# Kernel optimization log

Hardware: AMD Instinct MI355X
Metric: run time of the kernel (lower is better)

The kernel has to match this reference:

```python
import jax, jax.numpy as jnp
import numpy as np
from jax import lax

LAM = 1.0
B, L = 64, 512
WORD_DIM, POS_DIM, HIDDEN = 256, 32, 768
D_E = 3 * WORD_DIM            # 768, Xe feature dim
D_P = 2 * POS_DIM + WORD_DIM  # 320, Xp feature dim

# fixed piecewise-pool mask table: row 0 = padding, rows 1..3 = segments
MASK_TABLE = jnp.array([[0, 0, 0], [1, 0, 0], [0, 1, 0], [0, 0, 1]], dtype=jnp.float32)


def setup_inputs() -> dict:
    key = jax.random.key(0)
    ks = jax.random.split(key, 9)
    s1 = 1.0 / np.sqrt(D_E)
    s2 = 1.0 / np.sqrt(D_P)
    sc = 1.0 / np.sqrt(D_E * 3)
    return {
        "Xp": jax.random.normal(ks[0], (B, L, D_P), jnp.float32),
        "Xe": jax.random.normal(ks[1], (B, L, D_E), jnp.float32),
        "X_mask": jax.random.randint(ks[2], (B, L), 0, 4, jnp.int32),
        "W1": jax.random.uniform(ks[3], (D_E, D_E), jnp.float32, -s1, s1),
        "b1": jax.random.uniform(ks[4], (D_E,), jnp.float32, -s1, s1),
        "W2": jax.random.uniform(ks[5], (D_E, D_P), jnp.float32, -s2, s2),
        "b2": jax.random.uniform(ks[6], (D_E,), jnp.float32, -s2, s2),
        "Wc": jax.random.uniform(ks[7], (HIDDEN, D_E, 3), jnp.float32, -sc, sc),
        "bc": jax.random.uniform(ks[8], (HIDDEN,), jnp.float32, -sc, sc),
    }


def _forward(Xp, Xe, W1, b1, W2, b2, Wc, bc, X_mask):
    # gated linear fusion of entity and position features
    A = jax.nn.sigmoid(jnp.einsum('bld,od->blo', Xe / LAM, W1) + b1)   # [B,L,D_E]
    X = A * Xe + (1.0 - A) * jnp.tanh(jnp.einsum('bld,od->blo', Xp, W2) + b2)
    # conv1d over length, padding=1 (same)
    x_ncl = jnp.transpose(X, (0, 2, 1))                                 # [B,D_E,L]
    y = lax.conv_general_dilated(x_ncl, Wc, window_strides=(1,),
                                 padding=((1, 1),),
                                 dimension_numbers=('NCH', 'OIH', 'NCH'))
    y = jnp.transpose(y + bc[None, :, None], (0, 2, 1))                 # [B,L,H]
    # piecewise max pooling: mask-multiply then max over L, per segment
    m = MASK_TABLE[X_mask]                                              # [B,L,3]
    pooled = jnp.stack([jnp.max(y * m[:, :, k:k + 1], axis=1) for k in range(3)],
                       axis=-1)                                         # [B,H,3]
    return jnp.tanh(pooled.reshape(-1, HIDDEN * 3))                     # [B,3H]


def reference(Xp, Xe, X_mask, W1, b1, W2, b2, Wc, bc):
    return _forward(Xp, Xe, W1, b1, W2, b2, Wc, bc, X_mask)
```

## Files before the change

kernel.cpp:

```cpp
#include <hip/hip_runtime.h>
#include <math.h>

#define DE 768
#define DP 320
#define HID 768
#define LL 512
#define BB 64
#define M_TOT (BB * LL)
#define HD (HID * DE)

typedef _Float16 half8 __attribute__((ext_vector_type(8)));
typedef _Float16 half4 __attribute__((ext_vector_type(4)));
typedef _Float16 half2v __attribute__((ext_vector_type(2)));
typedef float floatx4 __attribute__((ext_vector_type(4)));

__device__ __forceinline__ void gload16(const void* g, void* l) {
    __builtin_amdgcn_global_load_lds(
        (const __attribute__((address_space(1))) unsigned int*)g,
        (__attribute__((address_space(3))) unsigned int*)l, 16, 0, 0);
}

__device__ __forceinline__ float fast_sigmoid(float x) {
    return __builtin_amdgcn_rcpf(1.f + __expf(-x));
}
__device__ __forceinline__ float fast_tanh(float x) {
    return 2.f * __builtin_amdgcn_rcpf(1.f + __expf(-2.f * x)) - 1.f;
}

__device__ __forceinline__ unsigned fkey(float v) {
    unsigned u = __float_as_uint(v);
    return (u & 0x80000000u) ? ~u : (u | 0x80000000u);
}
__device__ __forceinline__ float funkey(unsigned k) {
    unsigned u = (k & 0x80000000u) ? (k & 0x7FFFFFFFu) : ~k;
    return __uint_as_float(u);
}

__global__ __launch_bounds__(256) void prep_all(
    const float* __restrict__ Xe, const float* __restrict__ W1,
    const float* __restrict__ W2, const float* __restrict__ Wc,
    _Float16* __restrict__ Xe_h, _Float16* __restrict__ W1_h,
    _Float16* __restrict__ W2_h, _Float16* __restrict__ WcT)
{
    const int bid = blockIdx.x, tid = threadIdx.x;
    if (bid < 24576) {
        int idx = bid * 256 + tid;
        float4 v = ((const float4*)Xe)[idx];
        half4 h = {(_Float16)v.x, (_Float16)v.y, (_Float16)v.z, (_Float16)v.w};
        *(half4*)&Xe_h[(size_t)idx * 4] = h;
    } else if (bid < 25152) {
        int idx = (bid - 24576) * 256 + tid;
        float4 v = ((const float4*)W1)[idx];
        half4 h = {(_Float16)v.x, (_Float16)v.y, (_Float16)v.z, (_Float16)v.w};
        *(half4*)&W1_h[(size_t)idx * 4] = h;
    } else if (bid < 25392) {
        int idx = (bid - 25152) * 256 + tid;
        float4 v = ((const float4*)W2)[idx];
        half4 h = {(_Float16)v.x, (_Float16)v.y, (_Float16)v.z, (_Float16)v.w};
        *(half4*)&W2_h[(size_t)idx * 4] = h;
    } else {
        int idx = (bid - 25392) * 256 + tid;
        float a = Wc[(size_t)idx * 3 + 0];
        float b = Wc[(size_t)idx * 3 + 1];
        float c = Wc[(size_t)idx * 3 + 2];
        WcT[idx]          = (_Float16)a;
        WcT[HD + idx]     = (_Float16)b;
        WcT[2 * HD + idx] = (_Float16)c;
    }
}

__global__ __launch_bounds__(256) void gate_kernel(
    const _Float16* __restrict__ Xe_h, const float* __restrict__ Xp,
    const _Float16* __restrict__ W1_h, const float* __restrict__ b1,
    const _Float16* __restrict__ W2_h, const float* __restrict__ b2,
    _Float16* __restrict__ Xout)
{
    __shared__ __align__(16) char smem[24576];
    _Float16 (*As)[32] = (_Float16 (*)[32])smem;
    float    (*Af)[32] = (float (*)[32])smem;
    _Float16 (*Bs)[32] = (_Float16 (*)[32])(smem + 16384);
    unsigned (*Ep)[132] = (unsigned (*)[132])smem;

    const int tid = threadIdx.x;
    const int lane = tid & 63, wid = tid >> 6;
    const int quad = lane >> 4, l15 = lane & 15;
    const int wm = (wid & 1) * 64, wn = (wid >> 1) * 64;
    const int m0 = blockIdx.y * 128, n0 = blockIdx.x * 128;
    const int i4 = lane >> 2, c8 = (lane & 3) * 8;
    const int c8x = c8 ^ ((i4 & 3) * 8);
    const int i8 = lane >> 3, c4 = (lane & 7) * 4;
    const int c4x = c4 ^ ((i8 & 3) * 8);
    const int rsw = (l15 & 3) * 8;

    floatx4 acc[4][4] = {};

    for (int k0 = 0; k0 < DP; k0 += 32) {
        __syncthreads();
        #pragma unroll
        for (int t = 0; t < 4; ++t) {
            int rb = wid * 32 + t * 8;
            gload16(&Xp[(size_t)(m0 + rb + i8) * DP + k0 + c4x], &Af[rb][0]);
        }
        #pragma unroll
        for (int t = 0; t < 2; ++t) {
            int rb = wid * 32 + t * 16;
            gload16(&W2_h[(size_t)(n0 + rb + i4) * DP + k0 + c8x], &Bs[rb][0]);
        }
        __syncthreads();
        half8 af[4], bf[4];
        #pragma unroll
        for (int i = 0; i < 4; ++i) {
            int row = wm + i * 16 + l15;
            int sb = (quad * 8) ^ rsw;
            float4 x0 = *(float4*)&Af[row][sb];
            float4 x1 = *(float4*)&Af[row][sb + 4];
            half8 h = {(_Float16)x0.x, (_Float16)x0.y, (_Float16)x0.z, (_Float16)x0.w,
                       (_Float16)x1.x, (_Float16)x1.y, (_Float16)x1.z, (_Float16)x1.w};
            af[i] = h;
        }
        #pragma unroll
        for (int j = 0; j < 4; ++j)
            bf[j] = *(half8*)&Bs[wn + j * 16 + l15][(quad * 8) ^ rsw];
        #pragma unroll
        for (int i = 0; i < 4; ++i)
            #pragma unroll
            for (int j = 0; j < 4; ++j)
                acc[i][j] = __builtin_amdgcn_mfma_f32_16x16x32_f16(af[i], bf[j], acc[i][j], 0, 0, 0);
    }

    half4 tpk[4][4];
    #pragma unroll
    for (int j = 0; j < 4; ++j) {
        float b2v = b2[n0 + wn + j * 16 + l15];
        #pragma unroll
        for (int i = 0; i < 4; ++i) {
            half4 h;
            #pragma unroll
            for (int r = 0; r < 4; ++r)
                h[r] = (_Float16)fast_tanh(acc[i][j][r] + b2v);
            tpk[i][j] = h;
            acc[i][j] = (floatx4){0.f, 0.f, 0.f, 0.f};
        }
    }

    for (int k0 = 0; k0 < DE; k0 += 32) {
        __syncthreads();
        #pragma unroll
        for (int t = 0; t < 2; ++t) {
            int rb = wid * 32 + t * 16;
            gload16(&Xe_h[(size_t)(m0 + rb + i4) * DE + k0 + c8x], &As[rb][0]);
            gload16(&W1_h[(size_t)(n0 + rb + i4) * DE + k0 + c8x], &Bs[rb][0]);
        }
        __syncthreads();
        half8 af[4], bf[4];
        #pragma unroll
        for (int i = 0; i < 4; ++i)
            af[i] = *(half8*)&As[wm + i * 16 + l15][(quad * 8) ^ rsw];
        #pragma unroll
        for (int j = 0; j < 4; ++j)
            bf[j] = *(half8*)&Bs[wn + j * 16 + l15][(quad * 8) ^ rsw];
        #pragma unroll
        for (int i = 0; i < 4; ++i)
            #pragma unroll
            for (int j = 0; j < 4; ++j)
                acc[i][j] = __builtin_amdgcn_mfma_f32_16x16x32_f16(af[i], bf[j], acc[i][j], 0, 0, 0);
    }

    float b1v[4];
    #pragma unroll
    for (int j = 0; j < 4; ++j) b1v[j] = b1[n0 + wn + j * 16 + l15];

    #pragma unroll
    for (int p = 0; p < 4; ++p) {
        __syncthreads();
        if ((wm >> 6) == (p >> 1)) {
            #pragma unroll
            for (int ii = 0; ii < 2; ++ii) {
                int i = (p & 1) * 2 + ii;
                #pragma unroll
                for (int j = 0; j < 4; ++j) {
                    int col = wn + j * 16 + l15;
                    #pragma unroll
                    for (int r = 0; r < 4; ++r) {
                        int row_l = ii * 16 + quad * 4 + r;
                        float g = fast_sigmoid(acc[i][j][r] + b1v[j]);
                        half2v gt;
                        gt[0] = (_Float16)g;
                        gt[1] = tpk[i][j][r];
                        Ep[row_l][col] = __builtin_bit_cast(unsigned, gt);
                    }
                }
            }
        }
        __syncthreads();
        #pragma unroll
        for (int q = 0; q < 4; ++q) {
            int row_l = q * 8 + (tid >> 5);
            int col = (tid & 31) * 4;
            uint4 w = *(const uint4*)&Ep[row_l][col];
            size_t goff = (size_t)(m0 + p * 32 + row_l) * DE + n0 + col;
            half4 xe4 = *(const half4*)&Xe_h[goff];
            half4 r4;
            #pragma unroll
            for (int e = 0; e < 4; ++e) {
                half2v gt = __builtin_bit_cast(half2v, (&w.x)[e]);
                float g = (float)gt[0], t = (float)gt[1];
                float xe = (float)xe4[e];
                r4[e] = (_Float16)(g * xe + (1.f - g) * t);
            }
            *(half4*)&Xout[goff] = r4;
        }
    }
}

__global__ __launch_bounds__(256) void conv_pool_kernel(
    const _Float16* __restrict__ X, const _Float16* __restrict__ WcT,
    const float* __restrict__ bc, const int* __restrict__ mask,
    unsigned* __restrict__ pool)
{
    __shared__ __align__(16) _Float16 As[144][32];
    __shared__ __align__(16) _Float16 Bs[3][128][32];
    __shared__ unsigned lpool[384];
    __shared__ int smask[128];
    __shared__ int anyNot[3];

    const int tid = threadIdx.x;
    const int lane = tid & 63, wid = tid >> 6;
    const int quad = lane >> 4, l15 = lane & 15;
    const int wm = (wid & 1) * 64, wn = (wid >> 1) * 64;
    const int m0 = blockIdx.y * 128, n0 = blockIdx.x * 128;
    const int b = m0 >> 9, l0 = m0 & 511;
    const int i4 = lane >> 2, c8 = (lane & 3) * 8;
    const int c8x = c8 ^ ((i4 & 3) * 8);
    const int rsw = (l15 & 3) * 8;

    if (tid < 3) anyNot[tid] = 0;
    for (int i = tid; i < 384; i += 256) lpool[i] = 0u;
    if (tid < 128) smask[tid] = mask[b * LL + l0 + tid];
    if (l0 == 0   && tid < 4) *(uint4*)&As[7][tid * 8]   = make_uint4(0u, 0u, 0u, 0u);
    if (l0 == 384 && tid < 4) *(uint4*)&As[136][tid * 8] = make_uint4(0u, 0u, 0u, 0u);
    __syncthreads();
    if (tid < 128) {
        int mv = smask[tid];
        if (mv != 1) atomicOr(&anyNot[0], 1);
        if (mv != 2) atomicOr(&anyNot[1], 1);
        if (mv != 3) atomicOr(&anyNot[2], 1);
    }

    floatx4 acc[4][4] = {};
    for (int k0 = 0; k0 < DE; k0 += 32) {
        __syncthreads();
        #pragma unroll
        for (int t = 0; t < 2; ++t) {
            int c = wid + t * 4;
            int g = l0 - 8 + c * 16 + i4;
            if ((unsigned)g < (unsigned)LL)
                gload16(&X[((size_t)b * LL + g) * DE + k0 + c8x], &As[c * 16][0]);
        }
        if (wid == 0) {
            int g = l0 + 120 + i4;
            if ((unsigned)g < (unsigned)LL)
                gload16(&X[((size_t)b * LL + g) * DE + k0 + c8x], &As[128][0]);
        }
        #pragma unroll
        for (int s = 0; s < 3; ++s) {
            #pragma unroll
            for (int t = 0; t < 2; ++t) {
                int rb = wid * 32 + t * 16;
                gload16(&WcT[(size_t)s * HD + (size_t)(n0 + rb + i4) * DE + k0 + c8x],
                        &Bs[s][rb][0]);
            }
        }
        __syncthreads();
        #pragma unroll
        for (int s = 0; s < 3; ++s) {
            half8 af[4], bf[4];
            #pragma unroll
            for (int i = 0; i < 4; ++i) {
                int pr = wm + i * 16 + l15 + s + 7;
                af[i] = *(half8*)&As[pr][(quad * 8) ^ ((pr & 3) * 8)];
            }
            #pragma unroll
            for (int j = 0; j < 4; ++j)
                bf[j] = *(half8*)&Bs[s][wn + j * 16 + l15][(quad * 8) ^ rsw];
            #pragma unroll
            for (int i = 0; i < 4; ++i)
                #pragma unroll
                for (int j = 0; j < 4; ++j)
                    acc[i][j] = __builtin_amdgcn_mfma_f32_16x16x32_f16(af[i], bf[j], acc[i][j], 0, 0, 0);
        }
    }

    float tmax[4][3];
    #pragma unroll
    for (int j = 0; j < 4; ++j)
        #pragma unroll
        for (int sg = 0; sg < 3; ++sg) tmax[j][sg] = -1e38f;

    #pragma unroll
    for (int i = 0; i < 4; ++i) {
        #pragma unroll
        for (int r = 0; r < 4; ++r) {
            int ll = wm + i * 16 + quad * 4 + r;
            int seg = smask[ll] - 1;
            if (seg >= 0) {
                #pragma unroll
                for (int j = 0; j < 4; ++j)
                    tmax[j][seg] = fmaxf(tmax[j][seg], acc[i][j][r]);
            }
        }
    }
    #pragma unroll
    for (int j = 0; j < 4; ++j) {
        int h = wn + j * 16 + l15;
        float bias = bc[n0 + h];
        #pragma unroll
        for (int sg = 0; sg < 3; ++sg)
            if (tmax[j][sg] > -1e37f)
                atomicMax(&lpool[h * 3 + sg], fkey(tmax[j][sg] + bias));
    }
    __syncthreads();
    for (int i = tid; i < 384; i += 256) {
        int hl = i / 3, k = i - hl * 3;
        unsigned key = lpool[i];
        if (anyNot[k]) {
            unsigned z = fkey(0.0f);
            if (z > key) key = z;
        }
        atomicMax(&pool[((size_t)b * HID + n0 + hl) * 3 + k], key);
    }
}

__global__ void finish_k(const unsigned* __restrict__ pool, float* __restrict__ out) {
    int idx = blockIdx.x * blockDim.x + threadIdx.x;
    if (idx < BB * HID * 3) out[idx] = tanhf(funkey(pool[idx]));
}

extern "C" void kernel_launch(void* const* d_in, const int* in_sizes, int n_in,
                              void* d_out, int out_size, void* d_ws, size_t ws_size,
                              hipStream_t stream) {
    const float* Xp = (const float*)d_in[0];
    const float* Xe = (const float*)d_in[1];
    const int*   Xm = (const int*)d_in[2];
    const float* W1 = (const float*)d_in[3];
    const float* b1 = (const float*)d_in[4];
    const float* W2 = (const float*)d_in[5];
    const float* b2 = (const float*)d_in[6];
    const float* Wc = (const float*)d_in[7];
    const float* bc = (const float*)d_in[8];
    float* out = (float*)d_out;

    _Float16* Xe_h = (_Float16*)d_ws;
    _Float16* X_h  = Xe_h + (size_t)M_TOT * DE;
    _Float16* W1_h = X_h + (size_t)M_TOT * DE;
    _Float16* W2_h = W1_h + (size_t)DE * DE;
    _Float16* WcT  = W2_h + (size_t)DE * DP;
    unsigned* pool = (unsigned*)(WcT + (size_t)3 * HD);

    hipMemsetAsync(pool, 0, (size_t)BB * HID * 3 * sizeof(unsigned), stream);
    prep_all<<<27696, 256, 0, stream>>>(Xe, W1, W2, Wc, Xe_h, W1_h, W2_h, WcT);
    gate_kernel<<<dim3(DE / 128, M_TOT / 128), 256, 0, stream>>>(
        Xe_h, Xp, W1_h, b1, W2_h, b2, X_h);
    conv_pool_kernel<<<dim3(HID / 128, M_TOT / 128), 256, 0, stream>>>(
        X_h, WcT, bc, Xm, pool);
    finish_k<<<(BB * HID * 3 + 255) / 256, 256, 0, stream>>>(pool, out);
}
```

Before: 457.8 us.

## Drop Xe fp16 prepass, remap blocks per XCD, enlarge conv tile to 256 rows

Removes the separate Xe fp32-to-fp16 conversion pass. The gate kernel now loads fp32 Xe straight into LDS and converts it while building fragments, with a new swizzle for fp32 tiles. Block indices are remapped so neighbouring M tiles land on the same XCD, which should improve L2 reuse of weights and activations. The conv/pool kernel grows to 512 threads with a 256-row M tile, so each weight tile is reused across more rows and fewer blocks merge results through atomics. In exchange, the gate kernel moves twice the bytes through LDS for its Xe operand, and the conv kernel needs more LDS per block.

```diff
diff --git a/kernel.cpp b/kernel.cpp
--- a/kernel.cpp
+++ b/kernel.cpp
@@ -36,30 +36,25 @@
     return __uint_as_float(u);
 }
 
-__global__ __launch_bounds__(256) void prep_all(
-    const float* __restrict__ Xe, const float* __restrict__ W1,
-    const float* __restrict__ W2, const float* __restrict__ Wc,
-    _Float16* __restrict__ Xe_h, _Float16* __restrict__ W1_h,
-    _Float16* __restrict__ W2_h, _Float16* __restrict__ WcT)
+__global__ __launch_bounds__(256) void prep_w(
+    const float* __restrict__ W1, const float* __restrict__ W2,
+    const float* __restrict__ Wc,
+    _Float16* __restrict__ W1_h, _Float16* __restrict__ W2_h,
+    _Float16* __restrict__ WcT)
 {
     const int bid = blockIdx.x, tid = threadIdx.x;
-    if (bid < 24576) {
+    if (bid < 576) {
         int idx = bid * 256 + tid;
-        float4 v = ((const float4*)Xe)[idx];
-        half4 h = {(_Float16)v.x, (_Float16)v.y, (_Float16)v.z, (_Float16)v.w};
-        *(half4*)&Xe_h[(size_t)idx * 4] = h;
-    } else if (bid < 25152) {
-        int idx = (bid - 24576) * 256 + tid;
         float4 v = ((const float4*)W1)[idx];
         half4 h = {(_Float16)v.x, (_Float16)v.y, (_Float16)v.z, (_Float16)v.w};
         *(half4*)&W1_h[(size_t)idx * 4] = h;
-    } else if (bid < 25392) {
-        int idx = (bid - 25152) * 256 + tid;
+    } else if (bid < 816) {
+        int idx = (bid - 576) * 256 + tid;
         float4 v = ((const float4*)W2)[idx];
         half4 h = {(_Float16)v.x, (_Float16)v.y, (_Float16)v.z, (_Float16)v.w};
         *(half4*)&W2_h[(size_t)idx * 4] = h;
     } else {
-        int idx = (bid - 25392) * 256 + tid;
+        int idx = (bid - 816) * 256 + tid;
         float a = Wc[(size_t)idx * 3 + 0];
         float b = Wc[(size_t)idx * 3 + 1];
         float c = Wc[(size_t)idx * 3 + 2];
@@ -70,13 +65,12 @@
 }
 
 __global__ __launch_bounds__(256) void gate_kernel(
-    const _Float16* __restrict__ Xe_h, const float* __restrict__ Xp,
+    const float* __restrict__ Xe, const float* __restrict__ Xp,
     const _Float16* __restrict__ W1_h, const float* __restrict__ b1,
     const _Float16* __restrict__ W2_h, const float* __restrict__ b2,
     _Float16* __restrict__ Xout)
 {
     __shared__ __align__(16) char smem[24576];
-    _Float16 (*As)[32] = (_Float16 (*)[32])smem;
     float    (*Af)[32] = (float (*)[32])smem;
     _Float16 (*Bs)[32] = (_Float16 (*)[32])(smem + 16384);
     unsigned (*Ep)[132] = (unsigned (*)[132])smem;
@@ -85,11 +79,14 @@
     const int lane = tid & 63, wid = tid >> 6;
     const int quad = lane >> 4, l15 = lane & 15;
     const int wm = (wid & 1) * 64, wn = (wid >> 1) * 64;
-    const int m0 = blockIdx.y * 128, n0 = blockIdx.x * 128;
+    const int linear = blockIdx.y * 6 + blockIdx.x;
+    const int xcd = linear & 7, kk = linear >> 3;
+    const int n0 = (kk % 6) * 128;
+    const int m0 = (xcd * 32 + kk / 6) * 128;
     const int i4 = lane >> 2, c8 = (lane & 3) * 8;
     const int c8x = c8 ^ ((i4 & 3) * 8);
     const int i8 = lane >> 3, c4 = (lane & 7) * 4;
-    const int c4x = c4 ^ ((i8 & 3) * 8);
+    const int c4x = c4 ^ ((i8 & 7) * 4);
     const int rsw = (l15 & 3) * 8;
 
     floatx4 acc[4][4] = {};
@@ -110,10 +107,9 @@
         half8 af[4], bf[4];
         #pragma unroll
         for (int i = 0; i < 4; ++i) {
-            int row = wm + i * 16 + l15;
-            int sb = (quad * 8) ^ rsw;
-            float4 x0 = *(float4*)&Af[row][sb];
-            float4 x1 = *(float4*)&Af[row][sb + 4];
+            int row = wm + i * 16 + l15, r7 = row & 7;
+            float4 x0 = *(float4*)&Af[row][((2 * quad) ^ r7) * 4];
+            float4 x1 = *(float4*)&Af[row][((2 * quad + 1) ^ r7) * 4];
             half8 h = {(_Float16)x0.x, (_Float16)x0.y, (_Float16)x0.z, (_Float16)x0.w,
                        (_Float16)x1.x, (_Float16)x1.y, (_Float16)x1.z, (_Float16)x1.w};
             af[i] = h;
@@ -146,16 +142,26 @@
     for (int k0 = 0; k0 < DE; k0 += 32) {
         __syncthreads();
         #pragma unroll
+        for (int t = 0; t < 4; ++t) {
+            int rb = wid * 32 + t * 8;
+            gload16(&Xe[(size_t)(m0 + rb + i8) * DE + k0 + c4x], &Af[rb][0]);
+        }
+        #pragma unroll
         for (int t = 0; t < 2; ++t) {
             int rb = wid * 32 + t * 16;
-            gload16(&Xe_h[(size_t)(m0 + rb + i4) * DE + k0 + c8x], &As[rb][0]);
             gload16(&W1_h[(size_t)(n0 + rb + i4) * DE + k0 + c8x], &Bs[rb][0]);
         }
         __syncthreads();
         half8 af[4], bf[4];
         #pragma unroll
-        for (int i = 0; i < 4; ++i)
-            af[i] = *(half8*)&As[wm + i * 16 + l15][(quad * 8) ^ rsw];
+        for (int i = 0; i < 4; ++i) {
+            int row = wm + i * 16 + l15, r7 = row & 7;
+            float4 x0 = *(float4*)&Af[row][((2 * quad) ^ r7) * 4];
+            float4 x1 = *(float4*)&Af[row][((2 * quad + 1) ^ r7) * 4];
+            half8 h = {(_Float16)x0.x, (_Float16)x0.y, (_Float16)x0.z, (_Float16)x0.w,
+                       (_Float16)x1.x, (_Float16)x1.y, (_Float16)x1.z, (_Float16)x1.w};
+            af[i] = h;
+        }
         #pragma unroll
         for (int j = 0; j < 4; ++j)
             bf[j] = *(half8*)&Bs[wn + j * 16 + l15][(quad * 8) ^ rsw];
@@ -199,13 +205,13 @@
             int col = (tid & 31) * 4;
             uint4 w = *(const uint4*)&Ep[row_l][col];
             size_t goff = (size_t)(m0 + p * 32 + row_l) * DE + n0 + col;
-            half4 xe4 = *(const half4*)&Xe_h[goff];
+            float4 xe4 = *(const float4*)&Xe[goff];
             half4 r4;
             #pragma unroll
             for (int e = 0; e < 4; ++e) {
                 half2v gt = __builtin_bit_cast(half2v, (&w.x)[e]);
                 float g = (float)gt[0], t = (float)gt[1];
-                float xe = (float)xe4[e];
+                float xe = (&xe4.x)[e];
                 r4[e] = (_Float16)(g * xe + (1.f - g) * t);
             }
             *(half4*)&Xout[goff] = r4;
@@ -213,34 +219,37 @@
     }
 }
 
-__global__ __launch_bounds__(256) void conv_pool_kernel(
+__global__ __launch_bounds__(512) void conv_pool_kernel(
     const _Float16* __restrict__ X, const _Float16* __restrict__ WcT,
     const float* __restrict__ bc, const int* __restrict__ mask,
     unsigned* __restrict__ pool)
 {
-    __shared__ __align__(16) _Float16 As[144][32];
+    __shared__ __align__(16) _Float16 As[272][32];
     __shared__ __align__(16) _Float16 Bs[3][128][32];
     __shared__ unsigned lpool[384];
-    __shared__ int smask[128];
+    __shared__ int smask[256];
     __shared__ int anyNot[3];
 
     const int tid = threadIdx.x;
     const int lane = tid & 63, wid = tid >> 6;
     const int quad = lane >> 4, l15 = lane & 15;
-    const int wm = (wid & 1) * 64, wn = (wid >> 1) * 64;
-    const int m0 = blockIdx.y * 128, n0 = blockIdx.x * 128;
+    const int wm = (wid & 3) * 64, wn = (wid >> 2) * 64;
+    const int linear = blockIdx.y * 6 + blockIdx.x;
+    const int xcd = linear & 7, kk = linear >> 3;
+    const int n0 = (kk % 6) * 128;
+    const int m0 = (xcd * 16 + kk / 6) * 256;
     const int b = m0 >> 9, l0 = m0 & 511;
     const int i4 = lane >> 2, c8 = (lane & 3) * 8;
     const int c8x = c8 ^ ((i4 & 3) * 8);
     const int rsw = (l15 & 3) * 8;
 
     if (tid < 3) anyNot[tid] = 0;
-    for (int i = tid; i < 384; i += 256) lpool[i] = 0u;
-    if (tid < 128) smask[tid] = mask[b * LL + l0 + tid];
+    for (int i = tid; i < 384; i += 512) lpool[i] = 0u;
+    if (tid < 256) smask[tid] = mask[b * LL + l0 + tid];
     if (l0 == 0   && tid < 4) *(uint4*)&As[7][tid * 8]   = make_uint4(0u, 0u, 0u, 0u);
-    if (l0 == 384 && tid < 4) *(uint4*)&As[136][tid * 8] = make_uint4(0u, 0u, 0u, 0u);
+    if (l0 == 256 && tid < 4) *(uint4*)&As[264][tid * 8] = make_uint4(0u, 0u, 0u, 0u);
     __syncthreads();
-    if (tid < 128) {
+    if (tid < 256) {
         int mv = smask[tid];
         if (mv != 1) atomicOr(&anyNot[0], 1);
         if (mv != 2) atomicOr(&anyNot[1], 1);
@@ -252,24 +261,22 @@
         __syncthreads();
         #pragma unroll
         for (int t = 0; t < 2; ++t) {
-            int c = wid + t * 4;
+            int c = wid + t * 8;
             int g = l0 - 8 + c * 16 + i4;
             if ((unsigned)g < (unsigned)LL)
                 gload16(&X[((size_t)b * LL + g) * DE + k0 + c8x], &As[c * 16][0]);
         }
         if (wid == 0) {
-            int g = l0 + 120 + i4;
+            int g = l0 + 248 + i4;
             if ((unsigned)g < (unsigned)LL)
-                gload16(&X[((size_t)b * LL + g) * DE + k0 + c8x], &As[128][0]);
-        }
-        #pragma unroll
-        for (int s = 0; s < 3; ++s) {
-            #pragma unroll
-            for (int t = 0; t < 2; ++t) {
-                int rb = wid * 32 + t * 16;
-                gload16(&WcT[(size_t)s * HD + (size_t)(n0 + rb + i4) * DE + k0 + c8x],
-                        &Bs[s][rb][0]);
-            }
+                gload16(&X[((size_t)b * LL + g) * DE + k0 + c8x], &As[256][0]);
+        }
+        #pragma unroll
+        for (int t = 0; t < 3; ++t) {
+            int c = wid * 3 + t;
+            int s = c >> 3, rb = (c & 7) * 16;
+            gload16(&WcT[(size_t)s * HD + (size_t)(n0 + rb + i4) * DE + k0 + c8x],
+                    &Bs[s][rb][0]);
         }
         __syncthreads();
         #pragma unroll
@@ -320,7 +327,7 @@
                 atomicMax(&lpool[h * 3 + sg], fkey(tmax[j][sg] + bias));
     }
     __syncthreads();
-    for (int i = tid; i < 384; i += 256) {
+    for (int i = tid; i < 384; i += 512) {
         int hl = i / 3, k = i - hl * 3;
         unsigned key = lpool[i];
         if (anyNot[k]) {
@@ -350,18 +357,17 @@
     const float* bc = (const float*)d_in[8];
     float* out = (float*)d_out;
 
-    _Float16* Xe_h = (_Float16*)d_ws;
-    _Float16* X_h  = Xe_h + (size_t)M_TOT * DE;
+    _Float16* X_h  = (_Float16*)d_ws;
     _Float16* W1_h = X_h + (size_t)M_TOT * DE;
     _Float16* W2_h = W1_h + (size_t)DE * DE;
     _Float16* WcT  = W2_h + (size_t)DE * DP;
     unsigned* pool = (unsigned*)(WcT + (size_t)3 * HD);
 
     hipMemsetAsync(pool, 0, (size_t)BB * HID * 3 * sizeof(unsigned), stream);
-    prep_all<<<27696, 256, 0, stream>>>(Xe, W1, W2, Wc, Xe_h, W1_h, W2_h, WcT);
-    gate_kernel<<<dim3(DE / 128, M_TOT / 128), 256, 0, stream>>>(
-        Xe_h, Xp, W1_h, b1, W2_h, b2, X_h);
-    conv_pool_kernel<<<dim3(HID / 128, M_TOT / 128), 256, 0, stream>>>(
+    prep_w<<<3120, 256, 0, stream>>>(W1, W2, Wc, W1_h, W2_h, WcT);
+    gate_kernel<<<dim3(6, 256), 256, 0, stream>>>(
+        Xe, Xp, W1_h, b1, W2_h, b2, X_h);
+    conv_pool_kernel<<<dim3(6, 128), 512, 0, stream>>>(
         X_h, WcT, bc, Xm, pool);
     finish_k<<<(BB * HID * 3 + 255) / 256, 256, 0, stream>>>(pool, out);
 }
```

Result: slower. 550.6 us (+20.3%).
